# Optimization experiments

Measured on AMD Instinct MI355X. Metric: run time of the kernel, lower is better.

Reference implementation:

```python
import jax, jax.numpy as jnp
import numpy as np

K, D, N = 256, 1000, 65536


def setup_inputs() -> dict:
    key = jax.random.key(0)
    k1, k2 = jax.random.split(key)
    encoder_embedding = jax.random.normal(k1, (N, D), dtype=jnp.float32)
    # matches torch init: uniform_(-1/K, 1/D)
    weight = jax.random.uniform(k2, (K, D), dtype=jnp.float32, minval=-1.0 / K, maxval=1.0 / D)
    return {"encoder_embedding": encoder_embedding, "weight": weight}


def reference(encoder_embedding, weight):
    # squared L2 distance via expansion (same math as sum((x[:,None]-w)**2, -1)
    # without materializing the (N,K,D) broadcast intermediate)
    x_sq = jnp.sum(encoder_embedding * encoder_embedding, axis=1, keepdims=True)  # (N,1)
    w_sq = jnp.sum(weight * weight, axis=1)                                       # (K,)
    cross = encoder_embedding @ weight.T                                          # (N,K)
    distance = x_sq - 2.0 * cross + w_sq                                          # (N,K)
    idx = jnp.argmin(distance, axis=1)                                            # (N,)
    return weight[idx]                                                            # (N,D)
```

## Files before the change

kernel.cpp:

```cpp
#include <hip/hip_runtime.h>
#include <stdint.h>

#define N_ROWS 65536
#define DIM    1000
#define KCB    256

#define RB     64
#define DT     32
#define PITCH  36

__global__ __launch_bounds__(256) void wsq_old_kernel(const float* __restrict__ w,
                                                      float* __restrict__ wsq) {
    const int wave = threadIdx.x >> 6;
    const int lane = threadIdx.x & 63;
    const int k = blockIdx.x * 4 + wave;
    double s = 0.0;
    for (int c = lane; c < DIM / 4; c += 64) {
        const float4 v = *(const float4*)(w + k * DIM + c * 4);
        s += (double)v.x * v.x + (double)v.y * v.y + (double)v.z * v.z + (double)v.w * v.w;
    }
    #pragma unroll
    for (int off = 32; off; off >>= 1) s += __shfl_down(s, off, 64);
    if (lane == 0) wsq[k] = (float)s;
}

__global__ __launch_bounds__(256) void xsq_old_kernel(const float* __restrict__ x,
                                                      float* __restrict__ xsq) {
    const int wave = threadIdx.x >> 6;
    const int lane = threadIdx.x & 63;
    const int row = blockIdx.x * 4 + wave;
    double s = 0.0;
    for (int c = lane; c < DIM / 4; c += 64) {
        const float4 v = *(const float4*)(x + (size_t)row * DIM + c * 4);
        s += (double)v.x * v.x + (double)v.y * v.y + (double)v.z * v.z + (double)v.w * v.w;
    }
    #pragma unroll
    for (int off = 32; off; off >>= 1) s += __shfl_down(s, off, 64);
    if (lane == 0) xsq[row] = (float)s;
}

__global__ __launch_bounds__(256) void vq_old_kernel(const float* __restrict__ x,
                                                     const float* __restrict__ w,
                                                     const float* __restrict__ wsq,
                                                     const float* __restrict__ xsq,
                                                     float* __restrict__ out) {
    __shared__ float Xs[RB * PITCH];
    __shared__ float Ws[KCB * PITCH];
    __shared__ int   lidx[RB];

    const int tid  = threadIdx.x;
    const int row0 = blockIdx.x * RB;
    const int kt = tid & 31;
    const int rt = tid >> 5;

    double acc[8][8];
    #pragma unroll
    for (int i = 0; i < 8; i++)
        #pragma unroll
        for (int j = 0; j < 8; j++) acc[i][j] = 0.0;

    const int wk = tid >> 3;
    const int wg = tid & 7;
    const int xr = tid >> 2;
    const int xg = tid & 3;

    for (int d0 = 0; d0 < DIM; d0 += DT) {
        #pragma unroll
        for (int p = 0; p < 8; p++) {
            const int k = p * 32 + wk;
            const int d = d0 + wg * 4;
            float4 v = make_float4(0.f, 0.f, 0.f, 0.f);
            if (d < DIM) v = *(const float4*)(w + k * DIM + d);
            *(float4*)(&Ws[k * PITCH + wg * 4]) = v;
        }
        #pragma unroll
        for (int p = 0; p < 2; p++) {
            const int off = (xg + p * 4) * 4;
            const int d = d0 + off;
            float4 v = make_float4(0.f, 0.f, 0.f, 0.f);
            if (d < DIM) v = *(const float4*)(x + (size_t)(row0 + xr) * DIM + d);
            *(float4*)(&Xs[xr * PITCH + off]) = v;
        }
        __syncthreads();

        #pragma unroll
        for (int dq = 0; dq < DT; dq += 4) {
            float4 xf[8], wf[8];
            #pragma unroll
            for (int i = 0; i < 8; i++)
                xf[i] = *(const float4*)(&Xs[(rt + 8 * i) * PITCH + dq]);
            #pragma unroll
            for (int j = 0; j < 8; j++)
                wf[j] = *(const float4*)(&Ws[(kt + 32 * j) * PITCH + dq]);
            #pragma unroll
            for (int i = 0; i < 8; i++)
                #pragma unroll
                for (int j = 0; j < 8; j++) {
                    float p = xf[i].x * wf[j].x;
                    p = fmaf(xf[i].y, wf[j].y, p);
                    p = fmaf(xf[i].z, wf[j].z, p);
                    p = fmaf(xf[i].w, wf[j].w, p);
                    acc[i][j] += (double)p;
                }
        }
        __syncthreads();
    }

    #pragma unroll
    for (int i = 0; i < 8; i++) {
        const float xs = xsq[row0 + rt + 8 * i];
        float bestv = 3.4e38f;
        int   bestk = 0;
        #pragma unroll
        for (int j = 0; j < 8; j++) {
            const int k = kt + 32 * j;
            const float c32 = (float)acc[i][j];
            const float t1  = xs - 2.0f * c32;
            const float s   = t1 + wsq[k];
            if (s < bestv || (s == bestv && k < bestk)) { bestv = s; bestk = k; }
        }
        #pragma unroll
        for (int m = 16; m >= 1; m >>= 1) {
            const float ov = __shfl_xor(bestv, m, 64);
            const int   ok = __shfl_xor(bestk, m, 64);
            if (ov < bestv || (ov == bestv && ok < bestk)) { bestv = ov; bestk = ok; }
        }
        if (kt == 0) lidx[rt + 8 * i] = bestk;
    }
    __syncthreads();

    const int wave = tid >> 6;
    const int lane = tid & 63;
    for (int r = wave; r < RB; r += 4) {
        const int k = lidx[r];
        const float4* src = (const float4*)(w + k * DIM);
        float4* dst = (float4*)(out + (size_t)(row0 + r) * DIM);
        for (int c = lane; c < DIM / 4; c += 64) dst[c] = src[c];
    }
}


#define RBM    64
#define NSTEP  32
#define XHI    0
#define XLO    4096
#define WHIO   8192
#define WLOO   24576
#define LDSB   40960

typedef short bf16x8 __attribute__((ext_vector_type(8)));
typedef float f32x4  __attribute__((ext_vector_type(4)));
typedef unsigned short us8 __attribute__((ext_vector_type(8)));

__device__ __forceinline__ unsigned short f2bf(float f) {
    union { float f; unsigned int u; } v; v.f = f;
    return (unsigned short)((v.u + 0x7FFFu + ((v.u >> 16) & 1u)) >> 16);
}
__device__ __forceinline__ float bf2f(unsigned short h) {
    union { float f; unsigned int u; } v; v.u = ((unsigned int)h) << 16;
    return v.f;
}
__device__ __forceinline__ void glds16(const void* g, void* l) {
    __builtin_amdgcn_global_load_lds((const __attribute__((address_space(1))) unsigned int*)g,
                                     (__attribute__((address_space(3))) unsigned int*)l, 16, 0, 0);
}

__global__ __launch_bounds__(256) void prep_kernel(const float* __restrict__ w,
        float* __restrict__ wsq, unsigned short* __restrict__ whi, unsigned short* __restrict__ wlo,
        unsigned int* __restrict__ counter) {
    if (blockIdx.x == 0 && threadIdx.x == 0) counter[0] = 0;
    const int wave = threadIdx.x >> 6;
    const int lane = threadIdx.x & 63;
    const int k = blockIdx.x * 4 + wave;
    double s = 0.0;
    for (int c = lane; c < DIM / 4; c += 64) {
        const float4 v = *(const float4*)(w + k * DIM + c * 4);
        s += (double)v.x * v.x + (double)v.y * v.y + (double)v.z * v.z + (double)v.w * v.w;
    }
    #pragma unroll
    for (int off = 32; off; off >>= 1) s += __shfl_down(s, off, 64);
    if (lane == 0) wsq[k] = (float)s;

    const int ct = k >> 4, kl = k & 15;
    for (int c = lane; c < 256; c += 64) {
        float4 v = make_float4(0.f, 0.f, 0.f, 0.f);
        if (c < DIM / 4) v = *(const float4*)(w + k * DIM + c * 4);
        ushort4 h, l;
        h.x = f2bf(v.x); l.x = f2bf(v.x - bf2f(h.x));
        h.y = f2bf(v.y); l.y = f2bf(v.y - bf2f(h.y));
        h.z = f2bf(v.z); l.z = f2bf(v.z - bf2f(h.z));
        h.w = f2bf(v.w); l.w = f2bf(v.w - bf2f(h.w));
        const int step = c >> 3, qq = c & 7;
        const int pos = step * 16384 + ct * 1024 + ((qq >> 1) * 16 + kl) * 16 + (qq & 1) * 8;
        *(ushort4*)((char*)whi + pos) = h;
        *(ushort4*)((char*)wlo + pos) = l;
    }
}

__global__ __launch_bounds__(256) void xsq_s1_kernel(const float* __restrict__ x,
        float* __restrict__ xsq, float* __restrict__ s1) {
    const int wave = threadIdx.x >> 6;
    const int lane = threadIdx.x & 63;
    const int row = blockIdx.x * 4 + wave;
    double s = 0.0, a = 0.0;
    for (int c = lane; c < DIM / 4; c += 64) {
        const float4 v = *(const float4*)(x + (size_t)row * DIM + c * 4);
        s += (double)v.x * v.x + (double)v.y * v.y + (double)v.z * v.z + (double)v.w * v.w;
        a += (double)fabsf(v.x) + (double)fabsf(v.y) + (double)fabsf(v.z) + (double)fabsf(v.w);
    }
    #pragma unroll
    for (int off = 32; off; off >>= 1) { s += __shfl_down(s, off, 64); a += __shfl_down(a, off, 64); }
    if (lane == 0) { xsq[row] = (float)s; s1[row] = (float)a; }
}

__global__ __launch_bounds__(256, 2) void vq_main_kernel(
        const float* __restrict__ x, const float* __restrict__ w,
        const float* __restrict__ wsq, const float* __restrict__ xsq,
        const float* __restrict__ s1,
        const unsigned short* __restrict__ whi, const unsigned short* __restrict__ wlo,
        unsigned int* __restrict__ cmask, unsigned int* __restrict__ rlist,
        unsigned int* __restrict__ counter, float* __restrict__ out) {
    __shared__ __align__(16) char lds[2 * LDSB];
    const int tid  = threadIdx.x;
    const int lane = tid & 63;
    const int wv   = tid >> 6;
    const int row0 = blockIdx.x * RBM;

    const int srow = tid >> 2;
    const int sq0  = (tid & 3) * 2;
    const size_t xrow_off = (size_t)(row0 + srow) * DIM;
    const int xpos0 = (srow >> 4) * 1024 + ((sq0 >> 1) * 16 + (srow & 15)) * 16;

    f32x4 accm[4][4], accc[4][4];
    {
        const f32x4 z = {0.f, 0.f, 0.f, 0.f};
        #pragma unroll
        for (int i = 0; i < 4; i++)
            #pragma unroll
            for (int j = 0; j < 4; j++) { accm[i][j] = z; accc[i][j] = z; }
    }

    float4 xa, xb;
    auto xload = [&](int t) {
        const int dA = t * 32 + sq0 * 4, dB = dA + 4;
        xa = (dA <= DIM - 4) ? *(const float4*)(x + xrow_off + dA) : make_float4(0.f, 0.f, 0.f, 0.f);
        xb = (dB <= DIM - 4) ? *(const float4*)(x + xrow_off + dB) : make_float4(0.f, 0.f, 0.f, 0.f);
    };
    auto xwrite = [&](int b) {
        us8 h, l;
        h[0] = f2bf(xa.x); l[0] = f2bf(xa.x - bf2f(h[0]));
        h[1] = f2bf(xa.y); l[1] = f2bf(xa.y - bf2f(h[1]));
        h[2] = f2bf(xa.z); l[2] = f2bf(xa.z - bf2f(h[2]));
        h[3] = f2bf(xa.w); l[3] = f2bf(xa.w - bf2f(h[3]));
        h[4] = f2bf(xb.x); l[4] = f2bf(xb.x - bf2f(h[4]));
        h[5] = f2bf(xb.y); l[5] = f2bf(xb.y - bf2f(h[5]));
        h[6] = f2bf(xb.z); l[6] = f2bf(xb.z - bf2f(h[6]));
        h[7] = f2bf(xb.w); l[7] = f2bf(xb.w - bf2f(h[7]));
        *(us8*)(lds + b * LDSB + XHI + xpos0) = h;
        *(us8*)(lds + b * LDSB + XLO + xpos0) = l;
    };
    auto wstage = [&](int b, int t) {
        #pragma unroll
        for (int i = 0; i < 4; i++) {
            const int ch = wv * 4 + i;
            glds16(whi + (size_t)t * 8192 + ch * 512 + lane * 8, lds + b * LDSB + WHIO + ch * 1024);
            glds16(wlo + (size_t)t * 8192 + ch * 512 + lane * 8, lds + b * LDSB + WLOO + ch * 1024);
        }
    };
    auto compute = [&](int b) {
        const char* base = lds + b * LDSB;
        bf16x8 ahi[4], alo[4];
        #pragma unroll
        for (int rt = 0; rt < 4; rt++) {
            ahi[rt] = *(const bf16x8*)(base + XHI + rt * 1024 + lane * 16);
            alo[rt] = *(const bf16x8*)(base + XLO + rt * 1024 + lane * 16);
        }
        __builtin_amdgcn_s_setprio(1);
        #pragma unroll
        for (int jt = 0; jt < 4; jt++) {
            const int ct = wv * 4 + jt;
            const bf16x8 bhi = *(const bf16x8*)(base + WHIO + ct * 1024 + lane * 16);
            const bf16x8 blo = *(const bf16x8*)(base + WLOO + ct * 1024 + lane * 16);
            #pragma unroll
            for (int rt = 0; rt < 4; rt++) {
                accm[rt][jt] = __builtin_amdgcn_mfma_f32_16x16x32_bf16(ahi[rt], bhi, accm[rt][jt], 0, 0, 0);
                accc[rt][jt] = __builtin_amdgcn_mfma_f32_16x16x32_bf16(ahi[rt], blo, accc[rt][jt], 0, 0, 0);
                accc[rt][jt] = __builtin_amdgcn_mfma_f32_16x16x32_bf16(alo[rt], bhi, accc[rt][jt], 0, 0, 0);
            }
        }
        __builtin_amdgcn_s_setprio(0);
    };

    xload(0); wstage(0, 0); xwrite(0);
    __syncthreads();
    for (int t = 0; t < NSTEP; t++) {
        const int cur = t & 1;
        if (t + 1 < NSTEP) { xload(t + 1); wstage(1 - cur, t + 1); }
        compute(cur);
        if (t + 1 < NSTEP) xwrite(1 - cur);
        __syncthreads();
    }

    #pragma unroll
    for (int i = 0; i < 4; i++)
        #pragma unroll
        for (int j = 0; j < 4; j++) accm[i][j] += accc[i][j];

    const int g  = lane >> 4;
    const int cl = lane & 15;
    float* minw = (float*)lds;
    unsigned short* m16 = (unsigned short*)(lds + 1024);
    int* lidx = (int*)(lds + 3072);

    float wsqv[4];
    #pragma unroll
    for (int jt = 0; jt < 4; jt++) wsqv[jt] = wsq[wv * 64 + jt * 16 + cl];

    float xsv[4][4], mv[4][4];
    #pragma unroll
    for (int rt = 0; rt < 4; rt++)
        #pragma unroll
        for (int e = 0; e < 4; e++) {
            const int r = row0 + rt * 16 + g * 4 + e;
            const float xs = xsq[r];
            xsv[rt][e] = xs;
            mv[rt][e] = 2.5e-6f * s1[r] + 6e-7f * (xs + 64.0f) + 1e-12f;
        }

    #pragma unroll
    for (int rt = 0; rt < 4; rt++)
        #pragma unroll
        for (int jt = 0; jt < 4; jt++)
            #pragma unroll
            for (int e = 0; e < 4; e++) {
                const float c = accm[rt][jt][e];
                const float t1 = xsv[rt][e] - 2.0f * c;
                accm[rt][jt][e] = t1 + wsqv[jt];
            }

    #pragma unroll
    for (int rt = 0; rt < 4; rt++)
        #pragma unroll
        for (int e = 0; e < 4; e++) {
            float mn = fminf(fminf(accm[rt][0][e], accm[rt][1][e]), fminf(accm[rt][2][e], accm[rt][3][e]));
            #pragma unroll
            for (int m = 8; m; m >>= 1) mn = fminf(mn, __shfl_xor(mn, m, 64));
            if (cl == 0) minw[(rt * 16 + g * 4 + e) * 4 + wv] = mn;
        }
    __syncthreads();

    float tv[4][4];
    #pragma unroll
    for (int rt = 0; rt < 4; rt++)
        #pragma unroll
        for (int e = 0; e < 4; e++) {
            const int r = rt * 16 + g * 4 + e;
            const float gm = fminf(fminf(minw[r * 4 + 0], minw[r * 4 + 1]),
                                   fminf(minw[r * 4 + 2], minw[r * 4 + 3]));
            tv[rt][e] = gm + mv[rt][e];
        }
    #pragma unroll
    for (int rt = 0; rt < 4; rt++)
        #pragma unroll
        for (int jt = 0; jt < 4; jt++)
            #pragma unroll
            for (int e = 0; e < 4; e++) {
                const unsigned long long b = __ballot(accm[rt][jt][e] <= tv[rt][e]);
                if (cl == 0)
                    m16[(rt * 16 + g * 4 + e) * 16 + wv * 4 + jt] = (unsigned short)(b >> (g * 16));
            }
    __syncthreads();

    if (wv == 0) {
        unsigned int mw[8];
        int cnt = 0;
        #pragma unroll
        for (int i = 0; i < 8; i++) {
            mw[i] = (unsigned int)m16[lane * 16 + 2 * i] | ((unsigned int)m16[lane * 16 + 2 * i + 1] << 16);
            cnt += __popc(mw[i]);
        }
        int kb = 0;
        #pragma unroll
        for (int i = 7; i >= 0; i--) if (mw[i]) kb = 32 * i + __ffs(mw[i]) - 1;
        lidx[lane] = kb;
        unsigned int* mrow = cmask + (size_t)(row0 + lane) * 8;
        #pragma unroll
        for (int i = 0; i < 8; i++) mrow[i] = mw[i];

        const unsigned long long act = __ballot(cnt > 1);
        const int tot = __popcll(act);
        unsigned int basep = 0;
        if (lane == 0 && tot > 0) basep = atomicAdd(counter, (unsigned int)tot);
        basep = __shfl(basep, 0, 64);
        if (cnt > 1) {
            const int pfx = __popcll(act & ((1ull << lane) - 1ull));
            rlist[basep + pfx] = (unsigned int)(row0 + lane);
        }
    }
    __syncthreads();

    for (int r = wv; r < RBM; r += 4) {
        const int k = lidx[r];
        const float4* src = (const float4*)(w + (size_t)k * DIM);
        float4* dst = (float4*)(out + (size_t)(row0 + r) * DIM);
        for (int c = lane; c < DIM / 4; c += 64) dst[c] = src[c];
    }
}

__global__ __launch_bounds__(256) void resolve_kernel(const float* __restrict__ x,
        const float* __restrict__ w, const float* __restrict__ wsq,
        const float* __restrict__ xsq, const unsigned int* __restrict__ cmask,
        const unsigned int* __restrict__ rlist, const unsigned int* __restrict__ counter,
        float* __restrict__ out) {
    const int nact = (int)counter[0];
    const int wv   = threadIdx.x >> 6;
    const int lane = threadIdx.x & 63;
    const int nw   = gridDim.x * 4;

    for (int i = blockIdx.x * 4 + wv; i < nact; i += nw) {
        const int row = (int)rlist[i];
        unsigned int mw[8];
        #pragma unroll
        for (int q = 0; q < 8; q++) mw[q] = cmask[(size_t)row * 8 + q];

        float4 xq[4];
        #pragma unroll
        for (int p = 0; p < 4; p++) {
            const int c = lane + 64 * p;
            xq[p] = (c < DIM / 4) ? *(const float4*)(x + (size_t)row * DIM + c * 4)
                                  : make_float4(0.f, 0.f, 0.f, 0.f);
        }
        const float xs = xsq[row];
        float bv = 3.4e38f; int bk = KCB;
        for (int wd = 0; wd < 8; wd++) {
            unsigned int m = mw[wd];
            while (m) {
                const int k = wd * 32 + __ffs(m) - 1;
                m &= m - 1;
                double a = 0.0;
                #pragma unroll
                for (int p = 0; p < 4; p++) {
                    const int c = lane + 64 * p;
                    if (c < DIM / 4) {
                        const float4 wq = *(const float4*)(w + (size_t)k * DIM + c * 4);
                        float pt = xq[p].x * wq.x;
                        pt = fmaf(xq[p].y, wq.y, pt);
                        pt = fmaf(xq[p].z, wq.z, pt);
                        pt = fmaf(xq[p].w, wq.w, pt);
                        a += (double)pt;
                    }
                }
                #pragma unroll
                for (int off = 32; off; off >>= 1) a += __shfl_xor(a, off, 64);
                const float c32 = (float)a;
                const float t1 = xs - 2.0f * c32;
                const float sv = t1 + wsq[k];
                if (sv < bv) { bv = sv; bk = k; }
            }
        }
        const float4* src = (const float4*)(w + (size_t)bk * DIM);
        float4* dst = (float4*)(out + (size_t)row * DIM);
        for (int c = lane; c < DIM / 4; c += 64) dst[c] = src[c];
    }
}

extern "C" void kernel_launch(void* const* d_in, const int* in_sizes, int n_in,
                              void* d_out, int out_size, void* d_ws, size_t ws_size,
                              hipStream_t stream) {
    const float* x = (const float*)d_in[0];
    const float* w = (const float*)d_in[1];
    float* out  = (float*)d_out;
    float* base = (float*)d_ws;

    const size_t NEED = 983360ull * 4ull;
    if (ws_size < NEED) {
        float* wsq = base;
        float* xsq = wsq + KCB;
        wsq_old_kernel<<<KCB / 4, 256, 0, stream>>>(w, wsq);
        xsq_old_kernel<<<N_ROWS / 4, 256, 0, stream>>>(x, xsq);
        vq_old_kernel<<<N_ROWS / RB, 256, 0, stream>>>(x, w, wsq, xsq, out);
        return;
    }

    float*          wsq     = base;
    float*          xsq     = base + 256;
    float*          s1      = base + 65792;
    unsigned int*   counter = (unsigned int*)(base + 131328);
    unsigned int*   rlist   = (unsigned int*)(base + 131392);
    unsigned int*   cmask   = (unsigned int*)(base + 196928);
    unsigned short* whi     = (unsigned short*)(base + 721216);
    unsigned short* wlo     = (unsigned short*)(base + 852288);

    prep_kernel<<<KCB / 4, 256, 0, stream>>>(w, wsq, whi, wlo, counter);
    xsq_s1_kernel<<<N_ROWS / 4, 256, 0, stream>>>(x, xsq, s1);
    vq_main_kernel<<<N_ROWS / RBM, 256, 0, stream>>>(x, w, wsq, xsq, s1, whi, wlo,
                                                     cmask, rlist, counter, out);
    resolve_kernel<<<512, 256, 0, stream>>>(x, w, wsq, xsq, cmask, rlist, counter, out);
}
```

Before: 590.3 us.

## Fuse ambiguous-row resolve into main kernel and deepen x prefetch pipeline

Rows whose bf16 split-precision distances leave several candidate codewords are now resolved inside the main kernel. Candidate masks stay in LDS, so the global cmask/rlist/counter buffers, the atomic counter and the separate resolve kernel launch all go away, along with the second write of those rows' outputs. The x-tile load is restructured to use two register sets alternately, so global loads for step t+2 are issued while step t computes, and the staging lane mapping is changed. The cost is more register pressure, and the serial resolve work now stalls each block that has ambiguous rows.

```diff
diff --git a/kernel.cpp b/kernel.cpp
--- a/kernel.cpp
+++ b/kernel.cpp
@@ -166,9 +166,7 @@
 }
 
 __global__ __launch_bounds__(256) void prep_kernel(const float* __restrict__ w,
-        float* __restrict__ wsq, unsigned short* __restrict__ whi, unsigned short* __restrict__ wlo,
-        unsigned int* __restrict__ counter) {
-    if (blockIdx.x == 0 && threadIdx.x == 0) counter[0] = 0;
+        float* __restrict__ wsq, unsigned short* __restrict__ whi, unsigned short* __restrict__ wlo) {
     const int wave = threadIdx.x >> 6;
     const int lane = threadIdx.x & 63;
     const int k = blockIdx.x * 4 + wave;
@@ -218,18 +216,17 @@
         const float* __restrict__ wsq, const float* __restrict__ xsq,
         const float* __restrict__ s1,
         const unsigned short* __restrict__ whi, const unsigned short* __restrict__ wlo,
-        unsigned int* __restrict__ cmask, unsigned int* __restrict__ rlist,
-        unsigned int* __restrict__ counter, float* __restrict__ out) {
+        float* __restrict__ out) {
     __shared__ __align__(16) char lds[2 * LDSB];
     const int tid  = threadIdx.x;
     const int lane = tid & 63;
     const int wv   = tid >> 6;
     const int row0 = blockIdx.x * RBM;
 
-    const int srow = tid >> 2;
-    const int sq0  = (tid & 3) * 2;
+    const int qp   = (lane >> 4) & 3;
+    const int srow = wv * 16 + (lane & 15);
     const size_t xrow_off = (size_t)(row0 + srow) * DIM;
-    const int xpos0 = (srow >> 4) * 1024 + ((sq0 >> 1) * 16 + (srow & 15)) * 16;
+    const int xpos0 = wv * 1024 + lane * 16;
 
     f32x4 accm[4][4], accc[4][4];
     {
@@ -240,13 +237,18 @@
             for (int j = 0; j < 4; j++) { accm[i][j] = z; accc[i][j] = z; }
     }
 
-    float4 xa, xb;
-    auto xload = [&](int t) {
-        const int dA = t * 32 + sq0 * 4, dB = dA + 4;
-        xa = (dA <= DIM - 4) ? *(const float4*)(x + xrow_off + dA) : make_float4(0.f, 0.f, 0.f, 0.f);
-        xb = (dB <= DIM - 4) ? *(const float4*)(x + xrow_off + dB) : make_float4(0.f, 0.f, 0.f, 0.f);
+    float4 xa0, xb0, xa1, xb1;
+    auto xloadA = [&](int t) {
+        const int dA = t * 32 + qp * 8, dB = dA + 4;
+        xa0 = (dA <= DIM - 4) ? *(const float4*)(x + xrow_off + dA) : make_float4(0.f, 0.f, 0.f, 0.f);
+        xb0 = (dB <= DIM - 4) ? *(const float4*)(x + xrow_off + dB) : make_float4(0.f, 0.f, 0.f, 0.f);
     };
-    auto xwrite = [&](int b) {
+    auto xloadB = [&](int t) {
+        const int dA = t * 32 + qp * 8, dB = dA + 4;
+        xa1 = (dA <= DIM - 4) ? *(const float4*)(x + xrow_off + dA) : make_float4(0.f, 0.f, 0.f, 0.f);
+        xb1 = (dB <= DIM - 4) ? *(const float4*)(x + xrow_off + dB) : make_float4(0.f, 0.f, 0.f, 0.f);
+    };
+    auto xstore = [&](int b, const float4& xa, const float4& xb) {
         us8 h, l;
         h[0] = f2bf(xa.x); l[0] = f2bf(xa.x - bf2f(h[0]));
         h[1] = f2bf(xa.y); l[1] = f2bf(xa.y - bf2f(h[1]));
@@ -291,15 +293,29 @@
         __builtin_amdgcn_s_setprio(0);
     };
 
-    xload(0); wstage(0, 0); xwrite(0);
-    __syncthreads();
-    for (int t = 0; t < NSTEP; t++) {
-        const int cur = t & 1;
-        if (t + 1 < NSTEP) { xload(t + 1); wstage(1 - cur, t + 1); }
-        compute(cur);
-        if (t + 1 < NSTEP) xwrite(1 - cur);
+    wstage(0, 0);
+    xloadA(0); xstore(0, xa0, xb0);
+    xloadB(1);
+    __syncthreads();
+
+    for (int t = 0; t < 30; t += 2) {
+        xloadA(t + 2);
+        xstore(1 - (t & 1), xa1, xb1);
+        wstage(1 - (t & 1), t + 1);
+        compute(t & 1);
         __syncthreads();
-    }
+        xloadB(t + 3);
+        xstore(t & 1, xa0, xb0);
+        wstage(t & 1, t + 2);
+        compute(1 - (t & 1));
+        __syncthreads();
+    }
+    xstore(1, xa1, xb1);
+    wstage(1, 31);
+    compute(0);
+    __syncthreads();
+    compute(1);
+    __syncthreads();
 
     #pragma unroll
     for (int i = 0; i < 4; i++)
@@ -310,7 +326,9 @@
     const int cl = lane & 15;
     float* minw = (float*)lds;
     unsigned short* m16 = (unsigned short*)(lds + 1024);
-    int* lidx = (int*)(lds + 3072);
+    int* lidx   = (int*)(lds + 3072);
+    int* mlist  = (int*)(lds + 3328);
+    int* nmulti = (int*)(lds + 3584);
 
     float wsqv[4];
     #pragma unroll
@@ -383,54 +401,31 @@
         #pragma unroll
         for (int i = 7; i >= 0; i--) if (mw[i]) kb = 32 * i + __ffs(mw[i]) - 1;
         lidx[lane] = kb;
-        unsigned int* mrow = cmask + (size_t)(row0 + lane) * 8;
-        #pragma unroll
-        for (int i = 0; i < 8; i++) mrow[i] = mw[i];
-
         const unsigned long long act = __ballot(cnt > 1);
-        const int tot = __popcll(act);
-        unsigned int basep = 0;
-        if (lane == 0 && tot > 0) basep = atomicAdd(counter, (unsigned int)tot);
-        basep = __shfl(basep, 0, 64);
         if (cnt > 1) {
             const int pfx = __popcll(act & ((1ull << lane) - 1ull));
-            rlist[basep + pfx] = (unsigned int)(row0 + lane);
-        }
-    }
-    __syncthreads();
-
-    for (int r = wv; r < RBM; r += 4) {
-        const int k = lidx[r];
-        const float4* src = (const float4*)(w + (size_t)k * DIM);
-        float4* dst = (float4*)(out + (size_t)(row0 + r) * DIM);
-        for (int c = lane; c < DIM / 4; c += 64) dst[c] = src[c];
-    }
-}
-
-__global__ __launch_bounds__(256) void resolve_kernel(const float* __restrict__ x,
-        const float* __restrict__ w, const float* __restrict__ wsq,
-        const float* __restrict__ xsq, const unsigned int* __restrict__ cmask,
-        const unsigned int* __restrict__ rlist, const unsigned int* __restrict__ counter,
-        float* __restrict__ out) {
-    const int nact = (int)counter[0];
-    const int wv   = threadIdx.x >> 6;
-    const int lane = threadIdx.x & 63;
-    const int nw   = gridDim.x * 4;
-
-    for (int i = blockIdx.x * 4 + wv; i < nact; i += nw) {
-        const int row = (int)rlist[i];
+            mlist[pfx] = lane;
+        }
+        if (lane == 0) nmulti[0] = __popcll(act);
+    }
+    __syncthreads();
+
+    const int nm = nmulti[0];
+    for (int i = wv; i < nm; i += 4) {
+        const int r = mlist[i];
         unsigned int mw[8];
         #pragma unroll
-        for (int q = 0; q < 8; q++) mw[q] = cmask[(size_t)row * 8 + q];
+        for (int q = 0; q < 8; q++)
+            mw[q] = (unsigned int)m16[r * 16 + 2 * q] | ((unsigned int)m16[r * 16 + 2 * q + 1] << 16);
 
         float4 xq[4];
         #pragma unroll
         for (int p = 0; p < 4; p++) {
             const int c = lane + 64 * p;
-            xq[p] = (c < DIM / 4) ? *(const float4*)(x + (size_t)row * DIM + c * 4)
+            xq[p] = (c < DIM / 4) ? *(const float4*)(x + (size_t)(row0 + r) * DIM + c * 4)
                                   : make_float4(0.f, 0.f, 0.f, 0.f);
         }
-        const float xs = xsq[row];
+        const float xs = xsq[row0 + r];
         float bv = 3.4e38f; int bk = KCB;
         for (int wd = 0; wd < 8; wd++) {
             unsigned int m = mw[wd];
@@ -458,8 +453,14 @@
                 if (sv < bv) { bv = sv; bk = k; }
             }
         }
-        const float4* src = (const float4*)(w + (size_t)bk * DIM);
-        float4* dst = (float4*)(out + (size_t)row * DIM);
+        if (lane == 0) lidx[r] = bk;
+    }
+    __syncthreads();
+
+    for (int r = wv; r < RBM; r += 4) {
+        const int k = lidx[r];
+        const float4* src = (const float4*)(w + (size_t)k * DIM);
+        float4* dst = (float4*)(out + (size_t)(row0 + r) * DIM);
         for (int c = lane; c < DIM / 4; c += 64) dst[c] = src[c];
     }
 }
@@ -472,7 +473,7 @@
     float* out  = (float*)d_out;
     float* base = (float*)d_ws;
 
-    const size_t NEED = 983360ull * 4ull;
+    const size_t NEED = 393472ull * 4ull;
     if (ws_size < NEED) {
         float* wsq = base;
         float* xsq = wsq + KCB;
@@ -482,18 +483,13 @@
         return;
     }
 
-    float*          wsq     = base;
-    float*          xsq     = base + 256;
-    float*          s1      = base + 65792;
-    unsigned int*   counter = (unsigned int*)(base + 131328);
-    unsigned int*   rlist   = (unsigned int*)(base + 131392);
-    unsigned int*   cmask   = (unsigned int*)(base + 196928);
-    unsigned short* whi     = (unsigned short*)(base + 721216);
-    unsigned short* wlo     = (unsigned short*)(base + 852288);
-
-    prep_kernel<<<KCB / 4, 256, 0, stream>>>(w, wsq, whi, wlo, counter);
+    float*          wsq = base;
+    float*          xsq = base + 256;
+    float*          s1  = base + 65792;
+    unsigned short* whi = (unsigned short*)(base + 131328);
+    unsigned short* wlo = (unsigned short*)(base + 262400);
+
+    prep_kernel<<<KCB / 4, 256, 0, stream>>>(w, wsq, whi, wlo);
     xsq_s1_kernel<<<N_ROWS / 4, 256, 0, stream>>>(x, xsq, s1);
-    vq_main_kernel<<<N_ROWS / RBM, 256, 0, stream>>>(x, w, wsq, xsq, s1, whi, wlo,
-                                                     cmask, rlist, counter, out);
-    resolve_kernel<<<512, 256, 0, stream>>>(x, w, wsq, xsq, cmask, rlist, counter, out);
-}
+    vq_main_kernel<<<N_ROWS / RBM, 256, 0, stream>>>(x, w, wsq, xsq, s1, whi, wlo, out);
+}
```

Measured after the change: 572.1 us. 1.03x faster.
